# Performance work log

Hardware: AMD Instinct MI355X
Metric: run time of the kernel (lower is better)

## Reference

```python
import jax, jax.numpy as jnp
import numpy as np

B, S, E = 4, 2048, 1024


def setup_inputs() -> dict:
    key = jax.random.key(0)
    k1, k2, k3, k4 = jax.random.split(key, 4)
    scale = 1.0 / np.sqrt(E)
    return {
        "x": jax.random.normal(k1, (B, S, E), dtype=jnp.float32),
        "W_Q": jax.random.normal(k2, (E, E), dtype=jnp.float32) * scale,
        "W_K": jax.random.normal(k3, (E, E), dtype=jnp.float32) * scale,
        "W_V": jax.random.normal(k4, (E, E), dtype=jnp.float32) * scale,
    }


def reference(x, W_Q, W_K, W_V):
    # nn.Linear(E, E, bias=False): y = x @ W.T
    Q = jnp.einsum("bse,fe->bsf", x, W_Q)
    K = jnp.einsum("bse,fe->bsf", x, W_K)
    V = jnp.einsum("bse,fe->bsf", x, W_V)
    d = Q.shape[-1]
    scores = jnp.einsum("bqd,bkd->bqk", Q, K) / jnp.sqrt(jnp.float32(d))
    # causal mask: -inf strictly above the diagonal
    seq = Q.shape[1]
    causal = jnp.tril(jnp.ones((seq, seq), dtype=bool))  # [S,S]
    scores = jnp.where(causal[None, :, :], scores, jnp.float32(-jnp.inf))
    attn = jax.nn.softmax(scores, axis=-1)
    return jnp.einsum("bqk,bkd->bqd", attn, V)
```

## Files before the change

kernel.cpp:

```cpp
#include <hip/hip_runtime.h>
#include <hip/hip_bf16.h>
#include <stdint.h>

typedef __hip_bfloat16 bf16;
typedef __attribute__((ext_vector_type(8))) short bf16x8;
typedef __attribute__((ext_vector_type(4))) float f32x4;
typedef __attribute__((ext_vector_type(8))) unsigned short u16x8;
typedef __attribute__((ext_vector_type(4))) unsigned short u16x4;

#define SLEN 2048
#define ED   1024
#define NB   4
#define AS1 __attribute__((address_space(1)))
#define AS3 __attribute__((address_space(3)))
#define SB0() __builtin_amdgcn_sched_barrier(0)

static __device__ __forceinline__ unsigned short f2bf(float f) {
    return __builtin_bit_cast(unsigned short, __float2bfloat16(f));
}

__device__ __forceinline__ void gemm8p(
    const char* __restrict__ aT, int lda,
    const char* __restrict__ bT, int ldb,
    int nkt, char* sm, int tid, f32x4 (&acc)[8][4])
{
    const int lane = tid & 63, wave = tid >> 6;
    const int wm = wave >> 2, wn = wave & 3;
    const int fr = lane & 15, kc = lane >> 4;

    auto SU = [&](int isB, int kh, int Tn) {
        char* dst = sm + (Tn & 1) * 65536 + isB * 32768 + kh * 16384;
        const char* g = isB ? bT : aT;
        const int ld = isB ? ldb : lda;
#pragma unroll
        for (int j = 0; j < 2; ++j) {
            int rid = j * 512 + tid;
            int row = rid >> 2, c = rid & 3;
            const char* src = g + (size_t)row * ld + Tn * 128 + kh * 64
                            + ((c ^ ((row >> 1) & 3)) * 16);
            __builtin_amdgcn_global_load_lds(
                (const AS1 uint32_t*)src,
                (AS3 uint32_t*)(dst + (j * 512 + wave * 64) * 16), 16, 0, 0);
        }
    };
    auto RDA = [&](int T, int kh, bf16x8 (&a)[8]) {
        const char* pa = sm + (T & 1) * 65536 + kh * 16384;
#pragma unroll
        for (int i = 0; i < 8; ++i) {
            int row = wm * 128 + i * 16 + fr;
            a[i] = *(const bf16x8*)(pa + row * 64 + ((kc ^ ((row >> 1) & 3)) * 16));
        }
    };
    auto RDB = [&](int T, int kh, int nh, bf16x8 (&b)[2]) {
        const char* pb = sm + (T & 1) * 65536 + 32768 + kh * 16384;
#pragma unroll
        for (int n = 0; n < 2; ++n) {
            int row = wn * 64 + nh * 32 + n * 16 + fr;
            b[n] = *(const bf16x8*)(pb + row * 64 + ((kc ^ ((row >> 1) & 3)) * 16));
        }
    };
    auto MM = [&](bf16x8 (&a)[8], bf16x8 (&b)[2], int nh) {
        __builtin_amdgcn_s_setprio(1);
#pragma unroll
        for (int i = 0; i < 8; ++i)
#pragma unroll
            for (int n = 0; n < 2; ++n)
                acc[i][nh * 2 + n] = __builtin_amdgcn_mfma_f32_16x16x32_bf16(
                    a[i], b[n], acc[i][nh * 2 + n], 0, 0, 0);
        __builtin_amdgcn_s_setprio(0);
    };

    SU(0, 0, 0); SU(1, 0, 0); SU(0, 1, 0); SU(1, 1, 0);
    SU(0, 0, 1); SU(1, 0, 1); SU(0, 1, 1);
    asm volatile("s_waitcnt vmcnt(6)" ::: "memory");
    SB0();
    __builtin_amdgcn_s_barrier();

    for (int T = 0; T < nkt; ++T) {
        const bool p1 = (T + 1 < nkt), p2 = (T + 2 < nkt);
        bf16x8 a[8], b[2];
        RDA(T, 0, a); RDB(T, 0, 0, b);
        if (p1) SU(1, 1, T + 1);
        SB0(); __builtin_amdgcn_s_barrier();
        asm volatile("s_waitcnt lgkmcnt(0)" ::: "memory");
        SB0();
        MM(a, b, 0);
        SB0(); __builtin_amdgcn_s_barrier();
        RDB(T, 0, 1, b);
        if (p2) SU(0, 0, T + 2);
        SB0(); __builtin_amdgcn_s_barrier();
        asm volatile("s_waitcnt lgkmcnt(0)" ::: "memory");
        SB0();
        MM(a, b, 1);
        SB0(); __builtin_amdgcn_s_barrier();
        RDA(T, 1, a); RDB(T, 1, 0, b);
        if (p2) SU(1, 0, T + 2);
        SB0(); __builtin_amdgcn_s_barrier();
        asm volatile("s_waitcnt lgkmcnt(0)" ::: "memory");
        SB0();
        MM(a, b, 0);
        SB0(); __builtin_amdgcn_s_barrier();
        RDB(T, 1, 1, b);
        if (p2) SU(0, 1, T + 2);
        if (T < nkt - 2) asm volatile("s_waitcnt vmcnt(6)" ::: "memory");
        else             asm volatile("s_waitcnt vmcnt(0)" ::: "memory");
        SB0(); __builtin_amdgcn_s_barrier();
        asm volatile("s_waitcnt lgkmcnt(0)" ::: "memory");
        SB0();
        MM(a, b, 1);
        SB0(); __builtin_amdgcn_s_barrier();
    }
}

__device__ __forceinline__ void gemm_core8(
    const char* __restrict__ aT, int lda,
    const char* __restrict__ bT, int ldb,
    int nkt, char* sm, int tid, f32x4 (&acc)[4][4])
{
    const int lane = tid & 63, wave = tid >> 6;
    const int wm = wave >> 1, wn = wave & 1;
    const int fr = lane & 15, kc = lane >> 4;

    auto STAGE = [&](int kh, int Tn) {
        char* buf = sm + (Tn & 1) * 49152;
#pragma unroll
        for (int j = 0; j < 2; ++j) {
            int rid = j * 512 + tid;
            int row = rid >> 2, c = rid & 3;
            const char* src = aT + (size_t)row * lda + Tn * 128 + kh * 64
                            + ((c ^ ((row >> 1) & 3)) * 16);
            __builtin_amdgcn_global_load_lds(
                (const AS1 uint32_t*)src,
                (AS3 uint32_t*)(buf + kh * 16384 + (j * 512 + wave * 64) * 16),
                16, 0, 0);
        }
        {
            int row = tid >> 2, c = tid & 3;
            const char* src = bT + (size_t)row * ldb + Tn * 128 + kh * 64
                            + ((c ^ ((row >> 1) & 3)) * 16);
            __builtin_amdgcn_global_load_lds(
                (const AS1 uint32_t*)src,
                (AS3 uint32_t*)(buf + 32768 + kh * 8192 + (wave * 64) * 16),
                16, 0, 0);
        }
    };
    auto RD = [&](int T, int kh, bf16x8 (&a)[4], bf16x8 (&b)[4]) {
        const char* buf = sm + (T & 1) * 49152;
#pragma unroll
        for (int i = 0; i < 4; ++i) {
            int row = wm * 64 + i * 16 + fr;
            a[i] = *(const bf16x8*)(buf + kh * 16384 + row * 64
                                    + ((kc ^ ((row >> 1) & 3)) * 16));
        }
#pragma unroll
        for (int i = 0; i < 4; ++i) {
            int row = wn * 64 + i * 16 + fr;
            b[i] = *(const bf16x8*)(buf + 32768 + kh * 8192 + row * 64
                                    + ((kc ^ ((row >> 1) & 3)) * 16));
        }
    };
    auto MM = [&](bf16x8 (&a)[4], bf16x8 (&b)[4]) {
        __builtin_amdgcn_s_setprio(1);
#pragma unroll
        for (int i = 0; i < 4; ++i)
#pragma unroll
            for (int n = 0; n < 4; ++n)
                acc[i][n] = __builtin_amdgcn_mfma_f32_16x16x32_bf16(
                    a[i], b[n], acc[i][n], 0, 0, 0);
        __builtin_amdgcn_s_setprio(0);
    };

    STAGE(0, 0); STAGE(1, 0);
    asm volatile("s_waitcnt vmcnt(3)" ::: "memory");
    SB0();
    __builtin_amdgcn_s_barrier();

    bf16x8 aE[4], bE[4], aO[4], bO[4];
    for (int T = 0; T < nkt; ++T) {
        const bool pre = (T + 1 < nkt);
        RD(T, 0, aE, bE);
        SB0();
        if (pre) STAGE(0, T + 1);
        SB0();
        if (T > 0) {
            asm volatile("s_waitcnt lgkmcnt(8)" ::: "memory");
            SB0();
            MM(aO, bO);
        }
        if (pre) asm volatile("s_waitcnt vmcnt(3)" ::: "memory");
        else     asm volatile("s_waitcnt vmcnt(0)" ::: "memory");
        SB0();
        __builtin_amdgcn_s_barrier();
        RD(T, 1, aO, bO);
        SB0();
        if (pre) STAGE(1, T + 1);
        SB0();
        asm volatile("s_waitcnt lgkmcnt(8)" ::: "memory");
        SB0();
        MM(aE, bE);
        if (pre) asm volatile("s_waitcnt vmcnt(3)" ::: "memory");
        else     asm volatile("s_waitcnt vmcnt(0)" ::: "memory");
        SB0();
        __builtin_amdgcn_s_barrier();
    }
    asm volatile("s_waitcnt lgkmcnt(0)" ::: "memory");
    SB0();
    MM(aO, bO);
}

__global__ __launch_bounds__(256) void convert_to_bf16(
    const float* __restrict__ x, const float* __restrict__ wq,
    const float* __restrict__ wk, const float* __restrict__ wv,
    bf16* __restrict__ xb, bf16* __restrict__ wqb,
    bf16* __restrict__ wkb, bf16* __restrict__ wvb)
{
    long g = (long)blockIdx.x * 256 + threadIdx.x;
    const float* src; bf16* dst; long o;
    if (g < 1048576) { src = x; dst = xb; o = g * 8; }
    else {
        long g2 = g - 1048576;
        int w = (int)(g2 >> 17);
        o = (g2 & 131071) * 8;
        src = (w == 0) ? wq : (w == 1) ? wk : wv;
        dst = (w == 0) ? wqb : (w == 1) ? wkb : wvb;
    }
    float4 v0 = *(const float4*)(src + o);
    float4 v1 = *(const float4*)(src + o + 4);
    u16x8 r;
    r[0] = f2bf(v0.x); r[1] = f2bf(v0.y); r[2] = f2bf(v0.z); r[3] = f2bf(v0.w);
    r[4] = f2bf(v1.x); r[5] = f2bf(v1.y); r[6] = f2bf(v1.z); r[7] = f2bf(v1.w);
    *(u16x8*)(dst + o) = r;
}

__global__ __launch_bounds__(512, 2) void qkv_gemm(
    const bf16* __restrict__ xb, const bf16* __restrict__ wqb,
    const bf16* __restrict__ wkb, const bf16* __restrict__ wvb,
    bf16* __restrict__ Qb, bf16* __restrict__ Kb, bf16* __restrict__ Vt)
{
    extern __shared__ char smem[];
    int bid = blockIdx.x, tid = threadIdx.x;
    int lane = tid & 63, wave = tid >> 6;
    if (bid < 256) {
        int xcd = bid & 7, i = bid >> 3;
        int tm = (xcd << 2) | (i & 3);
        int tn = i >> 2;
        const bf16* W = (tn < 4) ? wqb : wkb;
        int tnl = tn & 3;
        f32x4 acc[8][4] = {};
        gemm8p((const char*)(xb + (size_t)tm * 256 * ED), ED * 2,
               (const char*)(W + (size_t)tnl * 256 * ED), ED * 2,
               16, smem, tid, acc);

        int wm = wave >> 2, wn = wave & 3;
        int rl = (lane >> 4) * 4, cl = lane & 15;
        bf16* C = (tn < 4) ? Qb : Kb;
#pragma unroll
        for (int mf = 0; mf < 8; ++mf)
#pragma unroll
            for (int j = 0; j < 4; ++j) {
                int r = tm * 256 + wm * 128 + mf * 16 + rl + j;
#pragma unroll
                for (int nf = 0; nf < 4; ++nf) {
                    int c = tnl * 256 + wn * 64 + nf * 16 + cl;
                    C[(size_t)r * ED + c] = __float2bfloat16(acc[mf][nf][j]);
                }
            }
    } else {
        int bid2 = bid - 256;
        int xcd = bid2 & 7, i = bid2 >> 3;
        int tm = (xcd << 2) | (i & 3);
        int tnl = i >> 2;
        f32x4 acc[4][4] = {};
        gemm_core8((const char*)(xb + (size_t)tm * 256 * ED), ED * 2,
                   (const char*)(wvb + (size_t)tnl * 128 * ED), ED * 2,
                   16, smem, tid, acc);

        int wm = wave >> 1, wn = wave & 1;
        int rl = (lane >> 4) * 4, cl = lane & 15;
#pragma unroll
        for (int mf = 0; mf < 4; ++mf)
#pragma unroll
            for (int j = 0; j < 4; ++j) {
                int r = tm * 256 + wm * 64 + mf * 16 + rl + j;
                int bb = r >> 11, s = r & 2047;
#pragma unroll
                for (int nf = 0; nf < 4; ++nf) {
                    int d = tnl * 128 + wn * 64 + nf * 16 + cl;
                    Vt[(((size_t)bb << 10) + d) * SLEN + s] = __float2bfloat16(acc[mf][nf][j]);
                }
            }
    }
}

__global__ __launch_bounds__(512, 2) void qk_gemm(
    const bf16* __restrict__ Qb, const bf16* __restrict__ Kb, float* __restrict__ Sc)
{
    extern __shared__ char smem[];
    int t = blockIdx.x, b = blockIdx.y, tid = threadIdx.x;
    int ti = 0;
    while ((ti + 1) * (ti + 2) / 2 <= t) ++ti;
    int tj = t - ti * (ti + 1) / 2;
    f32x4 acc[8][4] = {};
    gemm8p((const char*)(Qb + ((size_t)b * SLEN + ti * 256) * ED), ED * 2,
           (const char*)(Kb + ((size_t)b * SLEN + tj * 256) * ED), ED * 2,
           16, smem, tid, acc);

    float* Sb = Sc + (size_t)b * SLEN * SLEN;
    int lane = tid & 63, wave = tid >> 6, wm = wave >> 2, wn = wave & 3;
    int rl = (lane >> 4) * 4, cl = lane & 15;
#pragma unroll
    for (int mf = 0; mf < 8; ++mf)
#pragma unroll
        for (int j = 0; j < 4; ++j) {
            int r = ti * 256 + wm * 128 + mf * 16 + rl + j;
#pragma unroll
            for (int nf = 0; nf < 4; ++nf) {
                int c = tj * 256 + wn * 64 + nf * 16 + cl;
                Sb[(size_t)r * SLEN + c] = acc[mf][nf][j] * 0.03125f;
            }
        }
}

__global__ __launch_bounds__(256) void softmax_rows(float* __restrict__ Sc)
{
    int q = blockIdx.x, b = blockIdx.y, tid = threadIdx.x;
    float* row = Sc + ((size_t)b * SLEN + q) * SLEN;
    int lane = tid & 63, wave = tid >> 6;
    __shared__ float red[4];

    float vals[8];
    float lmax = -3.0e38f;
#pragma unroll
    for (int r = 0; r < 2; ++r) {
        int i4 = tid + r * 256;
        if (i4 * 4 <= q) {
            float4 v = *(const float4*)(row + i4 * 4);
            vals[r * 4 + 0] = v.x; vals[r * 4 + 1] = v.y;
            vals[r * 4 + 2] = v.z; vals[r * 4 + 3] = v.w;
#pragma unroll
            for (int e = 0; e < 4; ++e) {
                int k = i4 * 4 + e;
                if (k <= q) lmax = fmaxf(lmax, vals[r * 4 + e]);
            }
        }
    }
#pragma unroll
    for (int o = 32; o > 0; o >>= 1) lmax = fmaxf(lmax, __shfl_xor(lmax, o));
    if (lane == 0) red[wave] = lmax;
    __syncthreads();
    float m = fmaxf(fmaxf(red[0], red[1]), fmaxf(red[2], red[3]));
    __syncthreads();
    float lsum = 0.f;
#pragma unroll
    for (int r = 0; r < 2; ++r) {
        int i4 = tid + r * 256;
        if (i4 * 4 <= q)
#pragma unroll
            for (int e = 0; e < 4; ++e) {
                int k = i4 * 4 + e;
                if (k <= q) lsum += __expf(vals[r * 4 + e] - m);
            }
    }
#pragma unroll
    for (int o = 32; o > 0; o >>= 1) lsum += __shfl_xor(lsum, o);
    if (lane == 0) red[wave] = lsum;
    __syncthreads();
    float inv = 1.0f / (red[0] + red[1] + red[2] + red[3]);
    unsigned short* prow = (unsigned short*)row;
    int kmax = ((q >> 8) + 1) << 8;
#pragma unroll
    for (int r = 0; r < 2; ++r) {
        int i4 = tid + r * 256;
        if (i4 * 4 < kmax) {
            u16x4 o4;
#pragma unroll
            for (int e = 0; e < 4; ++e) {
                int k = i4 * 4 + e;
                float p = (k <= q) ? __expf(vals[r * 4 + e] - m) * inv : 0.0f;
                o4[e] = f2bf(p);
            }
            *(u16x4*)(prow + i4 * 4) = o4;
        }
    }
}

__global__ __launch_bounds__(512, 2) void pv_gemm(
    const bf16* __restrict__ P, const bf16* __restrict__ Vt, float* __restrict__ O)
{
    extern __shared__ char smem[];
    int mq = 7 - blockIdx.x, nd = blockIdx.y, b = blockIdx.z, tid = threadIdx.x;
    f32x4 acc[4][4] = {};
    int nkt = (mq + 1) * 4;
    gemm_core8((const char*)P + ((size_t)b * SLEN + mq * 256) * 8192, 8192,
               (const char*)(Vt + ((size_t)b * ED + nd * 128) * SLEN), SLEN * 2,
               nkt, smem, tid, acc);

    int lane = tid & 63, wave = tid >> 6, wm = wave >> 1, wn = wave & 1;
    int rl = (lane >> 4) * 4, cl = lane & 15;
    float* Ob = O + (size_t)b * SLEN * ED;
#pragma unroll
    for (int mf = 0; mf < 4; ++mf)
#pragma unroll
        for (int j = 0; j < 4; ++j) {
            int r = mq * 256 + wm * 64 + mf * 16 + rl + j;
#pragma unroll
            for (int nf = 0; nf < 4; ++nf) {
                int c = nd * 128 + wn * 64 + nf * 16 + cl;
                Ob[(size_t)r * ED + c] = acc[mf][nf][j];
            }
        }
}

extern "C" void kernel_launch(void* const* d_in, const int* in_sizes, int n_in,
                              void* d_out, int out_size, void* d_ws, size_t ws_size,
                              hipStream_t stream)
{
    const float* x  = (const float*)d_in[0];
    const float* wq = (const float*)d_in[1];
    const float* wk = (const float*)d_in[2];
    const float* wv = (const float*)d_in[3];
    float* out = (float*)d_out;

    char* ws = (char*)d_ws;
    bf16* xb  = (bf16*)(ws);
    bf16* wqb = (bf16*)(ws + 16777216);
    bf16* wkb = (bf16*)(ws + 18874368);
    bf16* wvb = (bf16*)(ws + 20971520);
    bf16* Qb  = (bf16*)(ws + 23068672);
    bf16* Kb  = (bf16*)(ws + 39845888);
    bf16* Vt  = (bf16*)(ws + 56623104);
    float* Sc = (float*)(ws + 73400320);

    (void)hipFuncSetAttribute((const void*)qkv_gemm,
            hipFuncAttributeMaxDynamicSharedMemorySize, 131072);
    (void)hipFuncSetAttribute((const void*)qk_gemm,
            hipFuncAttributeMaxDynamicSharedMemorySize, 131072);
    (void)hipFuncSetAttribute((const void*)pv_gemm,
            hipFuncAttributeMaxDynamicSharedMemorySize, 98304);

    convert_to_bf16<<<5632, 256, 0, stream>>>(x, wq, wk, wv, xb, wqb, wkb, wvb);
    qkv_gemm<<<512, 512, 131072, stream>>>(xb, wqb, wkb, wvb, Qb, Kb, Vt);
    qk_gemm<<<dim3(36, NB), 512, 131072, stream>>>(Qb, Kb, Sc);
    softmax_rows<<<dim3(SLEN, NB), 256, 0, stream>>>(Sc);
    pv_gemm<<<dim3(8, 8, NB), 512, 98304, stream>>>((const bf16*)Sc, Vt, out);
}
```

Baseline: 152.4 us.

## Split-K the two heaviest causal row-blocks in PV GEMM and reduce partials

The PV GEMM grid is rebuilt as a 1D launch. The two longest causal row-blocks (mq 6 and 7) are handled by 256x256 tiles with split-K into two halves, which write fp32 partials into reused workspace (the Q/K buffers). The remaining row-blocks keep the original 256x128 tiles. A new reduce_tail kernel sums the partials into the last 512 rows of each batch. This targets load imbalance from the triangular work, where the largest row-blocks set the tail latency, at the cost of an extra kernel launch and extra partial-sum traffic.

```diff
diff --git a/kernel.cpp b/kernel.cpp
--- a/kernel.cpp
+++ b/kernel.cpp
@@ -385,30 +385,78 @@
 }
 
 __global__ __launch_bounds__(512, 2) void pv_gemm(
-    const bf16* __restrict__ P, const bf16* __restrict__ Vt, float* __restrict__ O)
+    const bf16* __restrict__ P, const bf16* __restrict__ Vt,
+    float* __restrict__ O, float* __restrict__ pp0, float* __restrict__ pp1)
 {
     extern __shared__ char smem[];
-    int mq = 7 - blockIdx.x, nd = blockIdx.y, b = blockIdx.z, tid = threadIdx.x;
-    f32x4 acc[4][4] = {};
-    int nkt = (mq + 1) * 4;
-    gemm_core8((const char*)P + ((size_t)b * SLEN + mq * 256) * 8192, 8192,
-               (const char*)(Vt + ((size_t)b * ED + nd * 128) * SLEN), SLEN * 2,
+    int g = blockIdx.x, tid = threadIdx.x;
+    int lane = tid & 63, wave = tid >> 6;
+    if (g < 64) {
+        int mq = 7 - (g >> 5);
+        int w = g & 31;
+        int h = w & 1, b = (w >> 1) & 3, nd = (w >> 3) & 3;
+        int khalf = (mq == 7) ? 1024 : 896;
+        int nkt = khalf >> 6;
+        size_t koff = (size_t)h * khalf * 2;
+        f32x4 acc[8][4] = {};
+        gemm8p((const char*)P + ((size_t)b * SLEN + mq * 256) * 8192 + koff, 8192,
+               (const char*)(Vt + ((size_t)b * ED + nd * 256) * SLEN) + koff, SLEN * 2,
                nkt, smem, tid, acc);
 
-    int lane = tid & 63, wave = tid >> 6, wm = wave >> 1, wn = wave & 1;
-    int rl = (lane >> 4) * 4, cl = lane & 15;
-    float* Ob = O + (size_t)b * SLEN * ED;
-#pragma unroll
-    for (int mf = 0; mf < 4; ++mf)
-#pragma unroll
-        for (int j = 0; j < 4; ++j) {
-            int r = mq * 256 + wm * 64 + mf * 16 + rl + j;
-#pragma unroll
-            for (int nf = 0; nf < 4; ++nf) {
-                int c = nd * 128 + wn * 64 + nf * 16 + cl;
-                Ob[(size_t)r * ED + c] = acc[mf][nf][j];
-            }
-        }
+        int wm = wave >> 2, wn = wave & 3;
+        int rl = (lane >> 4) * 4, cl = lane & 15;
+        float* pp = h ? pp1 : pp0;
+#pragma unroll
+        for (int mf = 0; mf < 8; ++mf)
+#pragma unroll
+            for (int j = 0; j < 4; ++j) {
+                int r = mq * 256 + wm * 128 + mf * 16 + rl + j;
+#pragma unroll
+                for (int nf = 0; nf < 4; ++nf) {
+                    int c = nd * 256 + wn * 64 + nf * 16 + cl;
+                    pp[(((size_t)b << 9) + (r - 1536)) * ED + c] = acc[mf][nf][j];
+                }
+            }
+    } else {
+        int w = g - 64;
+        int mq = 5 - (w >> 5);
+        int b = w & 3, nd = (w >> 2) & 7;
+        f32x4 acc[4][4] = {};
+        int nkt = (mq + 1) * 4;
+        gemm_core8((const char*)P + ((size_t)b * SLEN + mq * 256) * 8192, 8192,
+                   (const char*)(Vt + ((size_t)b * ED + nd * 128) * SLEN), SLEN * 2,
+                   nkt, smem, tid, acc);
+
+        int wm = wave >> 1, wn = wave & 1;
+        int rl = (lane >> 4) * 4, cl = lane & 15;
+        float* Ob = O + (size_t)b * SLEN * ED;
+#pragma unroll
+        for (int mf = 0; mf < 4; ++mf)
+#pragma unroll
+            for (int j = 0; j < 4; ++j) {
+                int r = mq * 256 + wm * 64 + mf * 16 + rl + j;
+#pragma unroll
+                for (int nf = 0; nf < 4; ++nf) {
+                    int c = nd * 128 + wn * 64 + nf * 16 + cl;
+                    Ob[(size_t)r * ED + c] = acc[mf][nf][j];
+                }
+            }
+    }
+}
+
+__global__ __launch_bounds__(256) void reduce_tail(
+    const float* __restrict__ pp0, const float* __restrict__ pp1,
+    float* __restrict__ O)
+{
+    int t = blockIdx.x * 256 + threadIdx.x;
+    int b = t >> 17, rem = t & 131071;
+    const float4* p04 = (const float4*)pp0;
+    const float4* p14 = (const float4*)pp1;
+    float4* O4 = (float4*)O;
+    size_t pi = ((size_t)b << 17) + rem;
+    float4 a = p04[pi], c = p14[pi];
+    O4[((size_t)b * SLEN + 1536) * (ED / 4) + rem] =
+        make_float4(a.x + c.x, a.y + c.y, a.z + c.z, a.w + c.w);
 }
 
 extern "C" void kernel_launch(void* const* d_in, const int* in_sizes, int n_in,
@@ -430,17 +478,20 @@
     bf16* Kb  = (bf16*)(ws + 39845888);
     bf16* Vt  = (bf16*)(ws + 56623104);
     float* Sc = (float*)(ws + 73400320);
+    float* pp0 = (float*)(ws + 23068672);
+    float* pp1 = (float*)(ws + 39845888);
 
     (void)hipFuncSetAttribute((const void*)qkv_gemm,
             hipFuncAttributeMaxDynamicSharedMemorySize, 131072);
     (void)hipFuncSetAttribute((const void*)qk_gemm,
             hipFuncAttributeMaxDynamicSharedMemorySize, 131072);
     (void)hipFuncSetAttribute((const void*)pv_gemm,
-            hipFuncAttributeMaxDynamicSharedMemorySize, 98304);
+            hipFuncAttributeMaxDynamicSharedMemorySize, 131072);
 
     convert_to_bf16<<<5632, 256, 0, stream>>>(x, wq, wk, wv, xb, wqb, wkb, wvb);
     qkv_gemm<<<512, 512, 131072, stream>>>(xb, wqb, wkb, wvb, Qb, Kb, Vt);
     qk_gemm<<<dim3(36, NB), 512, 131072, stream>>>(Qb, Kb, Sc);
     softmax_rows<<<dim3(SLEN, NB), 256, 0, stream>>>(Sc);
-    pv_gemm<<<dim3(8, 8, NB), 512, 98304, stream>>>((const bf16*)Sc, Vt, out);
-}
+    pv_gemm<<<256, 512, 131072, stream>>>((const bf16*)Sc, Vt, out, pp0, pp1);
+    reduce_tail<<<2048, 256, 0, stream>>>(pp0, pp1, out);
+}
```

Result: no change. 154.1 us (+1.1%).
